# Kernel optimization log

Measured on AMD Instinct MI355X. Metric: run time of the kernel, lower is better.

The kernel has to match this reference:

```python
import jax, jax.numpy as jnp
import numpy as np
import math

B, S, INP = 64, 512, 64
D, H, L, DFF, LAT = 512, 8, 2, 2048, 128
SPARSE = 0.1  # sparse_factor default used by TransformerEncoderLayer


def _ln(x, g, b, eps=1e-5):
    m = x.mean(-1, keepdims=True)
    v = ((x - m) ** 2).mean(-1, keepdims=True)
    return (x - m) / jnp.sqrt(v + eps) * g + b


def _pe(s, d):
    pos = jnp.arange(s, dtype=jnp.float32)[:, None]
    div = jnp.exp(jnp.arange(0, d, 2, dtype=jnp.float32) * (-math.log(10000.0) / d))
    pe = jnp.zeros((s, d), dtype=jnp.float32)
    return pe.at[:, 0::2].set(jnp.sin(pos * div)).at[:, 1::2].set(jnp.cos(pos * div))


def _attn(h, g1, b1, wq, wk, wv, woW, wob):
    # h: (S, B, d). Faithful to source: transpose(1,2) yields (S, H, B, dk),
    # so attention is computed ACROSS THE BATCH axis at each timestep.
    s, bb, d = h.shape
    dk = d // H
    res = h
    hn = _ln(h, g1, b1)
    to_heads = lambda w: (hn @ w).reshape(s, bb, H, dk).swapaxes(1, 2)  # (S,H,B,dk)
    q, k, v = to_heads(wq), to_heads(wk), to_heads(wv)
    scores = jnp.einsum('shbd,shcd->shbc', q, k) / math.sqrt(dk)  # (S,H,B,B)
    kk = max(1, int(bb * SPARSE))  # topk row-sparsify before softmax
    thresh = jax.lax.top_k(scores, kk)[0][..., -1:]
    scores = jnp.where(scores >= thresh, scores, -1e9)
    w = jax.nn.softmax(scores, axis=-1)
    ctx = jnp.einsum('shbc,shcd->shbd', w, v).swapaxes(1, 2).reshape(s, bb, d)
    return ctx @ woW + wob + res


def _encoder(x, inW, inb, p):
    # x: (B, S, in_dim) -> (B, S, D)
    h = jnp.swapaxes(x, 0, 1)  # (S, B, in)
    h = (h @ inW + inb) * math.sqrt(D)
    h = h + _pe(h.shape[0], D)[:, None, :]
    for l in range(L):
        h = _attn(h, p['g1'][l], p['b1'][l], p['wq'][l], p['wk'][l], p['wv'][l], p['woW'][l], p['wob'][l])
        res = h
        f = _ln(h, p['g2'][l], p['b2'][l])
        f = jax.nn.gelu(f @ p['f1W'][l] + p['f1b'][l], approximate=False)
        h = f @ p['f2W'][l] + p['f2b'][l] + res
    h = _ln(h, p['gf'], p['bf'])
    return jnp.swapaxes(h, 0, 1)


_PKEYS = ['g1', 'b1', 'wq', 'wk', 'wv', 'woW', 'wob', 'g2', 'b2', 'f1W', 'f1b', 'f2W', 'f2b', 'gf', 'bf']


def _forward(x, enc_in_W, enc_in_b, enc_g1, enc_b1, enc_wq, enc_wk, enc_wv, enc_woW, enc_wob,
             enc_g2, enc_b2, enc_f1W, enc_f1b, enc_f2W, enc_f2b, enc_gf, enc_bf,
             mu_W, mu_b, lv_W, lv_b, dec_in_W, dec_in_b, dec_g1, dec_b1, dec_wq, dec_wk, dec_wv,
             dec_woW, dec_wob, dec_g2, dec_b2, dec_f1W, dec_f1b, dec_f2W, dec_f2b, dec_gf, dec_bf,
             out_W, out_b):
    enc_p = dict(zip(_PKEYS, [enc_g1, enc_b1, enc_wq, enc_wk, enc_wv, enc_woW, enc_wob, enc_g2, enc_b2, enc_f1W, enc_f1b, enc_f2W, enc_f2b, enc_gf, enc_bf]))
    dec_p = dict(zip(_PKEYS, [dec_g1, dec_b1, dec_wq, dec_wk, dec_wv, dec_woW, dec_wob, dec_g2, dec_b2, dec_f1W, dec_f1b, dec_f2W, dec_f2b, dec_gf, dec_bf]))
    enc_out = _encoder(x, enc_in_W, enc_in_b, enc_p)  # (B,S,D)
    pooled = enc_out.mean(axis=1)                      # (B,D)
    mu = pooled @ mu_W + mu_b
    logvar = pooled @ lv_W + lv_b
    z = mu  # eval mode: no reparameterization sampling
    z_seq = jnp.broadcast_to(z[:, None, :], (z.shape[0], S, LAT))
    dec_out = _encoder(z_seq, dec_in_W, dec_in_b, dec_p)
    recon = dec_out @ out_W + out_b
    return recon, mu, logvar


def setup_inputs() -> dict:
    key = jax.random.key(0)
    ks = iter(jax.random.split(key, 64))
    n = lambda shape, s=0.02: jax.random.normal(next(ks), shape, dtype=jnp.float32) * s

    def stack_params():
        return dict(
            g1=jnp.ones((L, D)), b1=jnp.zeros((L, D)),
            wq=n((L, D, D)), wk=n((L, D, D)), wv=n((L, D, D)),
            woW=n((L, D, D)), wob=jnp.zeros((L, D)),
            g2=jnp.ones((L, D)), b2=jnp.zeros((L, D)),
            f1W=n((L, D, DFF)), f1b=jnp.zeros((L, DFF)),
            f2W=n((L, DFF, D)), f2b=jnp.zeros((L, D)),
            gf=jnp.ones((D,)), bf=jnp.zeros((D,)))

    inp = {
        'x': jax.random.normal(next(ks), (B, S, INP), dtype=jnp.float32),
        'enc_in_W': n((INP, D), 0.05), 'enc_in_b': jnp.zeros((D,)),
        'mu_W': n((D, LAT), 0.05), 'mu_b': jnp.zeros((LAT,)),
        'lv_W': n((D, LAT), 0.05), 'lv_b': jnp.zeros((LAT,)),
        'dec_in_W': n((LAT, D), 0.05), 'dec_in_b': jnp.zeros((D,)),
        'out_W': n((D, INP), 0.05), 'out_b': jnp.zeros((INP,)),
    }
    for k_, v in stack_params().items():
        inp['enc_' + k_] = v
    for k_, v in stack_params().items():
        inp['dec_' + k_] = v
    return inp


def reference(x, enc_in_W, enc_in_b, enc_g1, enc_b1, enc_wq, enc_wk, enc_wv, enc_woW, enc_wob,
              enc_g2, enc_b2, enc_f1W, enc_f1b, enc_f2W, enc_f2b, enc_gf, enc_bf,
              mu_W, mu_b, lv_W, lv_b, dec_in_W, dec_in_b, dec_g1, dec_b1, dec_wq, dec_wk, dec_wv,
              dec_woW, dec_wob, dec_g2, dec_b2, dec_f1W, dec_f1b, dec_f2W, dec_f2b, dec_gf, dec_bf,
              out_W, out_b):
    return _forward(x, enc_in_W, enc_in_b, enc_g1, enc_b1, enc_wq, enc_wk, enc_wv, enc_woW, enc_wob,
                    enc_g2, enc_b2, enc_f1W, enc_f1b, enc_f2W, enc_f2b, enc_gf, enc_bf,
                    mu_W, mu_b, lv_W, lv_b, dec_in_W, dec_in_b, dec_g1, dec_b1, dec_wq, dec_wk, dec_wv,
                    dec_woW, dec_wob, dec_g2, dec_b2, dec_f1W, dec_f1b, dec_f2W, dec_f2b, dec_gf, dec_bf,
                    out_W, out_b)
```

## Files before the change

### kernel.cpp

```cpp
#include <hip/hip_runtime.h>
#include <math.h>


#define SQRT_D 22.62741699796952f
#define PE_C   0.017988946039015984f

typedef short frag8 __attribute__((ext_vector_type(8)));
typedef float accf4 __attribute__((ext_vector_type(4)));

#define GLL16(g, l) __builtin_amdgcn_global_load_lds( \
    (const __attribute__((address_space(1))) void*)(g), \
    (__attribute__((address_space(3))) void*)(l), 16, 0, 0)

__device__ __forceinline__ float bf2f(unsigned short u) {
    union { unsigned i; float f; } v; v.i = ((unsigned)u) << 16; return v.f;
}
__device__ __forceinline__ unsigned short f2bf(float f) {
    union { float f; unsigned i; } v; v.f = f;
    unsigned r = v.i + 0x7fff + ((v.i >> 16) & 1);
    return (unsigned short)(r >> 16);
}
__device__ __forceinline__ float pe_val(int s, int d) {
    float div = expf(-(float)(d & ~1) * PE_C);
    float ang = (float)s * div;
    return (d & 1) ? cosf(ang) : sinf(ang);
}
__device__ __forceinline__ float gelu_exact(float x) {
    return 0.5f * x * (1.0f + erff(x * 0.7071067811865476f));
}
__device__ __forceinline__ float gelu_fast(float x) {
    float xs = x * 0.7071067811865476f;
    float ax = fabsf(xs);
    float t  = 1.0f / (1.0f + 0.3275911f * ax);
    float p  = t * (0.254829592f + t * (-0.284496736f + t * (1.421413741f +
               t * (-1.453152027f + t * 1.061405429f))));
    float er = 1.0f - p * __expf(-ax * ax);
    er = (xs < 0.0f) ? -er : er;
    return 0.5f * x * (1.0f + er);
}

__device__ __forceinline__ void phase_bar() {
    __builtin_amdgcn_sched_barrier(0);
    __builtin_amdgcn_s_barrier();
    __builtin_amdgcn_sched_barrier(0);
}

__global__ __launch_bounds__(256) void pe_k(float* __restrict__ pe)
{
    const int s = blockIdx.x;
    const int d = threadIdx.x;
    pe[s * 512 + d]       = pe_val(s, d);
    pe[s * 512 + d + 256] = pe_val(s, d + 256);
}

__global__ __launch_bounds__(256) void embed_gemm_k(
    const float* __restrict__ x, const float* __restrict__ W,
    const float* __restrict__ bias, const float* __restrict__ pe,
    float* __restrict__ h)
{
    __shared__ float As[64][68];
    __shared__ float Ws[64][68];
    const int s = blockIdx.y;
    const int col0 = blockIdx.x * 64;
    const int tid = threadIdx.x;
#pragma unroll
    for (int i = 0; i < 16; i++) {
        int idx = i * 256 + tid;
        int r = idx >> 6, kk = idx & 63;
        As[kk][r] = x[((size_t)r * 512 + s) * 64 + kk];
        Ws[r][kk] = W[(size_t)r * 512 + col0 + kk];
    }
    __syncthreads();
    const int tm = (tid >> 4) << 2;
    const int tn = (tid & 15) << 2;
    float acc[4][4] = {};
#pragma unroll 8
    for (int kk = 0; kk < 64; kk++) {
        float4 a4 = *reinterpret_cast<const float4*>(&As[kk][tm]);
        float4 b4 = *reinterpret_cast<const float4*>(&Ws[kk][tn]);
        const float a[4] = {a4.x, a4.y, a4.z, a4.w};
        const float b[4] = {b4.x, b4.y, b4.z, b4.w};
#pragma unroll
        for (int i = 0; i < 4; i++)
#pragma unroll
            for (int j = 0; j < 4; j++)
                acc[i][j] += a[i] * b[j];
    }
    const int c = col0 + tn;
    float4 bi = *reinterpret_cast<const float4*>(&bias[c]);
    float4 pp = *reinterpret_cast<const float4*>(&pe[s * 512 + c]);
#pragma unroll
    for (int i = 0; i < 4; i++) {
        size_t row = ((size_t)s * 64 + tm + i) * 512;
        float4 o;
        o.x = (acc[i][0] + bi.x) * SQRT_D + pp.x;
        o.y = (acc[i][1] + bi.y) * SQRT_D + pp.y;
        o.z = (acc[i][2] + bi.z) * SQRT_D + pp.z;
        o.w = (acc[i][3] + bi.w) * SQRT_D + pp.w;
        *reinterpret_cast<float4*>(&h[row + c]) = o;
    }
}

__global__ __launch_bounds__(256) void dec_embed_k(
    const float* __restrict__ zemb, const float* __restrict__ pe,
    float* __restrict__ h)
{
    const int i4 = (blockIdx.x * 256 + threadIdx.x) * 4;
    const int d = i4 & 511;
    const int t = i4 >> 9;
    const int s = t >> 6, b = t & 63;
    float4 z = *reinterpret_cast<const float4*>(&zemb[b * 512 + d]);
    float4 p = *reinterpret_cast<const float4*>(&pe[s * 512 + d]);
    float4 o;
    o.x = z.x * SQRT_D + p.x;
    o.y = z.y * SQRT_D + p.y;
    o.z = z.z * SQRT_D + p.z;
    o.w = z.w * SQRT_D + p.w;
    *reinterpret_cast<float4*>(&h[i4]) = o;
}

__global__ __launch_bounds__(256) void stats_k(
    const float* __restrict__ x, float* __restrict__ st)
{
    const int row = blockIdx.x;
    const int tid = threadIdx.x;
    const float* xr = x + (size_t)row * 512;
    float2 vv = *reinterpret_cast<const float2*>(&xr[tid * 2]);
    float v0 = vv.x, v1 = vv.y;
    float ssum = v0 + v1;
#pragma unroll
    for (int off = 32; off > 0; off >>= 1) ssum += __shfl_down(ssum, off, 64);
    __shared__ float red[4];
    __shared__ float red2[4];
    const int wid = tid >> 6, lane = tid & 63;
    if (lane == 0) red[wid] = ssum;
    __syncthreads();
    float m = (red[0] + red[1] + red[2] + red[3]) * (1.f / 512.f);
    float d0 = v0 - m, d1 = v1 - m;
    float s2 = d0 * d0 + d1 * d1;
#pragma unroll
    for (int off = 32; off > 0; off >>= 1) s2 += __shfl_down(s2, off, 64);
    if (lane == 0) red2[wid] = s2;
    __syncthreads();
    if (tid == 0) {
        float var = (red2[0] + red2[1] + red2[2] + red2[3]) * (1.f / 512.f);
        st[row * 2]     = m;
        st[row * 2 + 1] = rsqrtf(var + 1e-5f);
    }
}

__global__ __launch_bounds__(256) void cast_ln_k(
    const float* __restrict__ x, const float* __restrict__ g,
    const float* __restrict__ b, unsigned short* __restrict__ y)
{
    const int row = blockIdx.x;
    const int tid = threadIdx.x;
    const float* xr = x + (size_t)row * 512;
    float2 vv = *reinterpret_cast<const float2*>(&xr[tid * 2]);
    float v0 = vv.x, v1 = vv.y;
    float ssum = v0 + v1;
#pragma unroll
    for (int off = 32; off > 0; off >>= 1) ssum += __shfl_down(ssum, off, 64);
    __shared__ float red[4];
    __shared__ float red2[4];
    const int wid = tid >> 6, lane = tid & 63;
    if (lane == 0) red[wid] = ssum;
    __syncthreads();
    float m = (red[0] + red[1] + red[2] + red[3]) * (1.f / 512.f);
    float d0 = v0 - m, d1 = v1 - m;
    float s2 = d0 * d0 + d1 * d1;
#pragma unroll
    for (int off = 32; off > 0; off >>= 1) s2 += __shfl_down(s2, off, 64);
    if (lane == 0) red2[wid] = s2;
    __syncthreads();
    float var = (red2[0] + red2[1] + red2[2] + red2[3]) * (1.f / 512.f);
    float rstd = rsqrtf(var + 1e-5f);
    float2 gg = *reinterpret_cast<const float2*>(&g[tid * 2]);
    float2 bb = *reinterpret_cast<const float2*>(&b[tid * 2]);
    ushort2 o;
    o.x = f2bf(d0 * rstd * gg.x + bb.x);
    o.y = f2bf(d1 * rstd * gg.y + bb.y);
    *reinterpret_cast<ushort2*>(&y[(size_t)row * 512 + tid * 2]) = o;
}

struct WTDesc { const float* src; unsigned short* dst; int Kd; int Nd; };

__global__ __launch_bounds__(256) void wtcast6_k(
    WTDesc d0, WTDesc d1, WTDesc d2, WTDesc d3, WTDesc d4, WTDesc d5)
{
    WTDesc d;
    switch (blockIdx.z) {
        case 0: d = d0; break; case 1: d = d1; break; case 2: d = d2; break;
        case 3: d = d3; break; case 4: d = d4; break; default: d = d5; break;
    }
    const int n0 = blockIdx.x * 32, k0 = blockIdx.y * 32;
    if (n0 >= d.Nd || k0 >= d.Kd) return;
    __shared__ float t[32][33];
    const int tx = threadIdx.x & 31, ty = threadIdx.x >> 5;
#pragma unroll
    for (int i = 0; i < 32; i += 8)
        t[ty + i][tx] = d.src[(size_t)(k0 + ty + i) * d.Nd + (n0 + tx)];
    __syncthreads();
#pragma unroll
    for (int i = 0; i < 32; i += 8)
        d.dst[(size_t)(n0 + ty + i) * d.Kd + (k0 + tx)] = f2bf(t[tx][ty + i]);
}

template<int ACT, int OUTBF, int RES, int BIAS>
__global__ __launch_bounds__(256, 2) void mgemm128_k(
    const unsigned short* __restrict__ A, int lda,
    const unsigned short* __restrict__ Bt, int ldb,
    const float* __restrict__ bias,
    const float* res, float* Cf, unsigned short* Cb, int ldc, int K)
{
    __shared__ unsigned short sm[32768];
    const int tid = threadIdx.x;
    const int wave = tid >> 6, lane = tid & 63;
    const int row0 = blockIdx.x * 128;
    const int col0 = blockIdx.y * 128;
    const int wr = wave >> 1, wc = wave & 1;
    const int wrbase = wr * 64, wcbase = wc * 64;
    const int frow = lane & 15;
    const int fcol = (lane >> 4) * 8;
    const int fxorE = (lane & 7) << 3;
    const int ccol = ((lane & 7) ^ (lane >> 3)) * 8;

    const int NT = K >> 6;

    auto stageA = [&](int buf, int k0t) {
#pragma unroll
        for (int i = 0; i < 4; i++) {
            int chunk = wave * 4 + i;
            GLL16(A + (size_t)(row0 + chunk * 8 + (lane >> 3)) * lda + k0t + ccol,
                  &sm[buf * 16384 + chunk * 512]);
        }
    };
    auto stageB = [&](int buf, int k0t) {
#pragma unroll
        for (int i = 0; i < 4; i++) {
            int chunk = wave * 4 + i;
            GLL16(Bt + (size_t)(col0 + chunk * 8 + (lane >> 3)) * ldb + k0t + ccol,
                  &sm[buf * 16384 + 8192 + chunk * 512]);
        }
    };

    accf4 acc[4][4] = {};
    frag8 af0[4], af1[4], bfr[4][2];

    stageA(0, 0); stageB(0, 0);
    if (NT > 1) { stageA(1, 64); stageB(1, 64); }
    if (NT > 1) asm volatile("s_waitcnt vmcnt(8)");
    else        asm volatile("s_waitcnt vmcnt(0)");
    phase_bar();

    for (int t = 0; t < NT; ++t) {
        const int ab = (t & 1) * 16384;
        const int bb = ab + 8192;
        const bool pf = (t + 2) < NT;
        const int kpf = (t + 2) << 6;

#pragma unroll
        for (int mi = 0; mi < 4; mi++)
            af0[mi] = *(const frag8*)&sm[ab + (wrbase + mi * 16 + frow) * 64 + (fcol ^ fxorE)];
#pragma unroll
        for (int nj = 0; nj < 4; nj++)
#pragma unroll
            for (int ks = 0; ks < 2; ks++)
                bfr[nj][ks] = *(const frag8*)&sm[bb + (wcbase + nj * 16 + frow) * 64 + ((ks * 32 + fcol) ^ fxorE)];
        phase_bar();
        __builtin_amdgcn_s_setprio(1);
#pragma unroll
        for (int mi = 0; mi < 4; mi++)
#pragma unroll
            for (int nj = 0; nj < 4; nj++)
                acc[mi][nj] = __builtin_amdgcn_mfma_f32_16x16x32_bf16(
                    bfr[nj][0], af0[mi], acc[mi][nj], 0, 0, 0);
        __builtin_amdgcn_s_setprio(0);
        phase_bar();

#pragma unroll
        for (int mi = 0; mi < 4; mi++)
            af1[mi] = *(const frag8*)&sm[ab + (wrbase + mi * 16 + frow) * 64 + ((32 + fcol) ^ fxorE)];
        if (pf) stageB(t & 1, kpf);
        phase_bar();
        __builtin_amdgcn_s_setprio(1);
#pragma unroll
        for (int mi = 0; mi < 4; mi++)
#pragma unroll
            for (int nj = 0; nj < 4; nj++)
                acc[mi][nj] = __builtin_amdgcn_mfma_f32_16x16x32_bf16(
                    bfr[nj][1], af1[mi], acc[mi][nj], 0, 0, 0);
        __builtin_amdgcn_s_setprio(0);
        if (pf) stageA(t & 1, kpf);
        if (pf) asm volatile("s_waitcnt vmcnt(8)");
        else    asm volatile("s_waitcnt vmcnt(0)");
        phase_bar();
    }

    const int lrow = lane & 15;
    const int lcol = (lane >> 4) * 4;
#pragma unroll
    for (int mi = 0; mi < 4; mi++) {
        const int r = row0 + wrbase + mi * 16 + lrow;
#pragma unroll
        for (int nj = 0; nj < 4; nj++) {
            const int c = col0 + wcbase + nj * 16 + lcol;
            float4 v = make_float4(acc[mi][nj][0], acc[mi][nj][1],
                                   acc[mi][nj][2], acc[mi][nj][3]);
            if (BIAS) {
                float4 bi = *reinterpret_cast<const float4*>(&bias[c]);
                v.x += bi.x; v.y += bi.y; v.z += bi.z; v.w += bi.w;
            }
            if (ACT) {
                v.x = gelu_fast(v.x); v.y = gelu_fast(v.y);
                v.z = gelu_fast(v.z); v.w = gelu_fast(v.w);
            }
            if (RES) {
                float4 rr = *reinterpret_cast<const float4*>(&res[(size_t)r * ldc + c]);
                v.x += rr.x; v.y += rr.y; v.z += rr.z; v.w += rr.w;
            }
            if (OUTBF) {
                ushort4 o;
                o.x = f2bf(v.x); o.y = f2bf(v.y); o.z = f2bf(v.z); o.w = f2bf(v.w);
                *reinterpret_cast<ushort4*>(&Cb[(size_t)r * ldc + c]) = o;
            } else {
                *reinterpret_cast<float4*>(&Cf[(size_t)r * ldc + c]) = v;
            }
        }
    }
}

__global__ __launch_bounds__(256) void attn2_k(
    const unsigned short* __restrict__ qkv, unsigned short* __restrict__ ctx)
{
    __shared__ float QT[64][68];
    __shared__ float KT[64][68];
    __shared__ float Vs[64][68];
    const int blk = blockIdx.x;
    const int sl = blk >> 3, hh = blk & 7;
    const int tid = threadIdx.x;
    const size_t qbase = (size_t)sl * 64 * 1536 + (size_t)hh * 64;
#pragma unroll
    for (int i = 0; i < 16; i++) {
        int idx = i * 256 + tid;
        int rr = idx >> 6, cc = idx & 63;
        const size_t g = qbase + (size_t)rr * 1536 + cc;
        QT[cc][rr] = bf2f(qkv[g]);
        KT[cc][rr] = bf2f(qkv[g + 512]);
        Vs[rr][cc] = bf2f(qkv[g + 1024]);
    }
    __syncthreads();
    const int tm = (tid >> 4) << 2;
    const int tn = (tid & 15) << 2;
    float sc[4][4] = {};
#pragma unroll 4
    for (int kk = 0; kk < 64; kk++) {
        float4 a4 = *reinterpret_cast<const float4*>(&QT[kk][tm]);
        float4 b4 = *reinterpret_cast<const float4*>(&KT[kk][tn]);
        const float a[4] = {a4.x, a4.y, a4.z, a4.w};
        const float b[4] = {b4.x, b4.y, b4.z, b4.w};
#pragma unroll
        for (int i = 0; i < 4; i++)
#pragma unroll
            for (int j = 0; j < 4; j++)
                sc[i][j] += a[i] * b[j];
    }
    __syncthreads();
    float (*ScT)[68] = KT;
#pragma unroll
    for (int i = 0; i < 4; i++)
#pragma unroll
        for (int j = 0; j < 4; j++)
            ScT[tn + j][tm + i] = sc[i][j] * 0.125f;
    __syncthreads();
    const int row = tid & 63, seg = tid >> 6;
    float* candp = &QT[0][0];
    {
        float top[6];
#pragma unroll
        for (int i = 0; i < 6; i++) top[i] = -3.4e38f;
#pragma unroll
        for (int c = seg * 16; c < seg * 16 + 16; c++) {
            float vv = ScT[c][row];
            if (vv > top[5]) {
                top[5] = vv;
#pragma unroll
                for (int i = 5; i > 0; i--)
                    if (top[i] > top[i - 1]) { float t = top[i]; top[i] = top[i - 1]; top[i - 1] = t; }
            }
        }
#pragma unroll
        for (int i = 0; i < 6; i++) candp[row * 24 + seg * 6 + i] = top[i];
    }
    __syncthreads();
    if (seg == 0) {
        float t6[6];
#pragma unroll
        for (int i = 0; i < 6; i++) t6[i] = -3.4e38f;
#pragma unroll
        for (int j = 0; j < 24; j++) {
            float vv = candp[row * 24 + j];
            if (vv > t6[5]) {
                t6[5] = vv;
#pragma unroll
                for (int i = 5; i > 0; i--)
                    if (t6[i] > t6[i - 1]) { float t = t6[i]; t6[i] = t6[i - 1]; t6[i - 1] = t; }
            }
        }
        ScT[row][64] = t6[5];
        ScT[row][65] = t6[0];
    }
    __syncthreads();
    {
        const float thresh = ScT[row][64], mx = ScT[row][65];
        float dsum = 0.f;
#pragma unroll
        for (int c = seg * 16; c < seg * 16 + 16; c++) {
            float vv = ScT[c][row];
            float w = (vv >= thresh) ? expf(vv - mx) : 0.f;
            dsum += w;
            QT[c][row] = w;
        }
        Vs[row][64 + seg] = dsum;
    }
    __syncthreads();
    {
        const float rd = 1.f / (Vs[row][64] + Vs[row][65] + Vs[row][66] + Vs[row][67]);
#pragma unroll
        for (int c = seg * 16; c < seg * 16 + 16; c++) QT[c][row] *= rd;
    }
    __syncthreads();
    {
        float acc[4][4] = {};
#pragma unroll 4
        for (int c = 0; c < 64; c++) {
            float4 p4 = *reinterpret_cast<const float4*>(&QT[c][tm]);
            float4 v4 = *reinterpret_cast<const float4*>(&Vs[c][tn]);
            const float p[4] = {p4.x, p4.y, p4.z, p4.w};
            const float b[4] = {v4.x, v4.y, v4.z, v4.w};
#pragma unroll
            for (int i = 0; i < 4; i++)
#pragma unroll
                for (int j = 0; j < 4; j++)
                    acc[i][j] += p[i] * b[j];
        }
#pragma unroll
        for (int i = 0; i < 4; i++) {
            ushort4 o;
            o.x = f2bf(acc[i][0]); o.y = f2bf(acc[i][1]);
            o.z = f2bf(acc[i][2]); o.w = f2bf(acc[i][3]);
            *reinterpret_cast<ushort4*>(
                &ctx[(size_t)(sl * 64 + tm + i) * 512 + hh * 64 + tn]) = o;
        }
    }
}

template<int ACT, int PERM, int LN>
__global__ __launch_bounds__(256) void gemm_k(
    const float* __restrict__ A, int lda,
    const float* __restrict__ W, int ldw,
    const float* __restrict__ bias,
    const float* res,
    float* C, int ldc,
    int K,
    const float* __restrict__ stats,
    const float* __restrict__ lng, const float* __restrict__ lnb)
{
    __shared__ float As[16][68];
    __shared__ float Ws[16][68];
    __shared__ float ms[64], rss[64];
    const int row0 = blockIdx.y * 64;
    const int col0 = blockIdx.x * 64;
    const int tid = threadIdx.x;
    if (LN) {
        if (tid < 64) {
            ms[tid]  = stats[(row0 + tid) * 2];
            rss[tid] = stats[(row0 + tid) * 2 + 1];
        }
        __syncthreads();
    }
    const int tm = (tid >> 4) << 2;
    const int tn = (tid & 15) << 2;
    float acc[4][4] = {};
    for (int k0 = 0; k0 < K; k0 += 16) {
#pragma unroll
        for (int i = 0; i < 4; i++) {
            int idx = i * 256 + tid;
            int r = idx >> 4, kk = idx & 15;
            float v = A[(size_t)(row0 + r) * lda + (k0 + kk)];
            if (LN) v = (v - ms[r]) * rss[r] * lng[k0 + kk] + lnb[k0 + kk];
            As[kk][r] = v;
        }
#pragma unroll
        for (int i = 0; i < 4; i++) {
            int idx = i * 256 + tid;
            int kk = idx >> 6, c = idx & 63;
            Ws[kk][c] = W[(size_t)(k0 + kk) * ldw + (col0 + c)];
        }
        __syncthreads();
#pragma unroll
        for (int kk = 0; kk < 16; kk++) {
            float4 a4 = *reinterpret_cast<const float4*>(&As[kk][tm]);
            float4 b4 = *reinterpret_cast<const float4*>(&Ws[kk][tn]);
            const float a[4] = {a4.x, a4.y, a4.z, a4.w};
            const float b[4] = {b4.x, b4.y, b4.z, b4.w};
#pragma unroll
            for (int i = 0; i < 4; i++)
#pragma unroll
                for (int j = 0; j < 4; j++)
                    acc[i][j] += a[i] * b[j];
        }
        __syncthreads();
    }
#pragma unroll
    for (int i = 0; i < 4; i++) {
        int r = row0 + tm + i;
#pragma unroll
        for (int j = 0; j < 4; j++) {
            int c = col0 + tn + j;
            float v = acc[i][j];
            if (bias) v += bias[c];
            if (ACT == 1) v = gelu_exact(v);
            if (res) v += res[(size_t)r * ldc + c];
            if (PERM) {
                int bb = r & 63, ss = r >> 6;
                C[((size_t)bb * 512 + ss) * ldc + c] = v;
            } else {
                C[(size_t)r * ldc + c] = v;
            }
        }
    }
}

__global__ __launch_bounds__(512) void pool_ln_k(
    const float* __restrict__ h, const float* __restrict__ st,
    const float* __restrict__ gf, const float* __restrict__ bf,
    float* __restrict__ pooled)
{
    const int b = blockIdx.x;
    const int d = threadIdx.x;
    const float g = gf[d], bb = bf[d];
    float acc = 0.f;
    for (int s = 0; s < 512; s++) {
        int r = s * 64 + b;
        float m = st[r * 2], rs = st[r * 2 + 1];
        acc += (h[(size_t)r * 512 + d] - m) * rs * g + bb;
    }
    pooled[b * 512 + d] = acc * (1.f / 512.f);
}

static void run_layer2(const float* const* p, int l,
                       float* h, unsigned short* hn_bf,
                       unsigned short* qkv, int chunk_rows,
                       unsigned short* f1c, int cw,
                       unsigned short* wqkv_t, unsigned short* wo_t,
                       unsigned short* f1_t, unsigned short* f2_t,
                       hipStream_t stream)
{
    const float* g1  = p[0] + l * 512;
    const float* b1  = p[1] + l * 512;
    const float* wq  = p[2] + (size_t)l * 262144;
    const float* wk  = p[3] + (size_t)l * 262144;
    const float* wv  = p[4] + (size_t)l * 262144;
    const float* wo  = p[5] + (size_t)l * 262144;
    const float* wob = p[6] + l * 512;
    const float* g2  = p[7] + l * 512;
    const float* b2  = p[8] + l * 512;
    const float* f1W = p[9] + (size_t)l * 1048576;
    const float* f1b = p[10] + l * 2048;
    const float* f2W = p[11] + (size_t)l * 1048576;
    const float* f2b = p[12] + l * 512;

    {
        WTDesc d0 = {wq,  wqkv_t,          512,  512};
        WTDesc d1 = {wk,  wqkv_t + 262144, 512,  512};
        WTDesc d2 = {wv,  wqkv_t + 524288, 512,  512};
        WTDesc d3 = {wo,  wo_t,            512,  512};
        WTDesc d4 = {f1W, f1_t,            512,  2048};
        WTDesc d5 = {f2W, f2_t,            2048, 512};
        wtcast6_k<<<dim3(64, 64, 6), 256, 0, stream>>>(d0, d1, d2, d3, d4, d5);
    }

    cast_ln_k<<<32768, 256, 0, stream>>>(h, g1, b1, hn_bf);
    for (int r0 = 0; r0 < 32768; r0 += chunk_rows) {
        mgemm128_k<0, 1, 0, 0><<<dim3(chunk_rows / 128, 12), 256, 0, stream>>>(
            hn_bf + (size_t)r0 * 512, 512, wqkv_t, 512, nullptr,
            nullptr, nullptr, qkv, 1536, 512);
        attn2_k<<<(chunk_rows / 64) * 8, 256, 0, stream>>>(
            qkv, hn_bf + (size_t)r0 * 512);
    }
    mgemm128_k<0, 0, 1, 1><<<dim3(256, 4), 256, 0, stream>>>(
        hn_bf, 512, wo_t, 512, wob, h, h, nullptr, 512, 512);

    cast_ln_k<<<32768, 256, 0, stream>>>(h, g2, b2, hn_bf);
    for (int c0 = 0; c0 < 2048; c0 += cw) {
        mgemm128_k<1, 1, 0, 1><<<dim3(256, cw / 128), 256, 0, stream>>>(
            hn_bf, 512, f1_t + (size_t)c0 * 512, 512, f1b + c0,
            nullptr, nullptr, f1c, cw, 512);
        if (c0 == 0)
            mgemm128_k<0, 0, 1, 1><<<dim3(256, 4), 256, 0, stream>>>(
                f1c, cw, f2_t + c0, 2048, f2b, h, h, nullptr, 512, cw);
        else
            mgemm128_k<0, 0, 1, 0><<<dim3(256, 4), 256, 0, stream>>>(
                f1c, cw, f2_t + c0, 2048, nullptr, h, h, nullptr, 512, cw);
    }
}

extern "C" void kernel_launch(void* const* d_in, const int* in_sizes, int n_in,
                              void* d_out, int out_size, void* d_ws, size_t ws_size,
                              hipStream_t stream)
{
    const float* x       = (const float*)d_in[0];
    const float* enc_inW = (const float*)d_in[1];
    const float* enc_inb = (const float*)d_in[2];
    const float* mu_W    = (const float*)d_in[3];
    const float* mu_b    = (const float*)d_in[4];
    const float* lv_W    = (const float*)d_in[5];
    const float* lv_b    = (const float*)d_in[6];
    const float* dec_inW = (const float*)d_in[7];
    const float* dec_inb = (const float*)d_in[8];
    const float* out_W   = (const float*)d_in[9];
    const float* out_b   = (const float*)d_in[10];
    const float* const* ep = (const float* const*)(d_in + 11);
    const float* const* dp = (const float* const*)(d_in + 26);

    float* fout   = (float*)d_out;
    float* mu_out = fout + 2097152;
    float* lv_out = mu_out + 8192;

    const size_t SZ = (size_t)32768 * 512;
    size_t off = 0;
    char* base = (char*)d_ws;
    auto take = [&](size_t bytes) -> char* {
        char* pp = base + off;
        off = (off + bytes + 255) & ~(size_t)255;
        return pp;
    };
    float*          h      = (float*)take(SZ * 4);
    unsigned short* hn_bf  = (unsigned short*)take(SZ * 2);
    unsigned short* wqkv_t = (unsigned short*)take(1536 * 512 * 2);
    unsigned short* wo_t   = (unsigned short*)take(512 * 512 * 2);
    unsigned short* f1_t   = (unsigned short*)take(2048 * 512 * 2);
    unsigned short* f2_t   = (unsigned short*)take(512 * 2048 * 2);
    float*          stats  = (float*)take(65536 * 4);
    float*          pooled = (float*)take(131072);
    float*          zemb   = (float*)take(131072);
    float*          pe     = (float*)take(512 * 512 * 4);

    unsigned short* qkv; unsigned short* f1c;
    int chunk_rows, cw;
    size_t rem = (ws_size > off) ? (ws_size - off) : 0;
    const size_t F1_FULL  = (size_t)32768 * 2048 * 2;
    const size_t QKV_FULL = (size_t)32768 * 1536 * 2;
    if (rem >= F1_FULL + 512) {
        unsigned short* share = (unsigned short*)take(F1_FULL);
        qkv = share; f1c = share; chunk_rows = 32768; cw = 2048;
    } else if (rem >= QKV_FULL + 512) {
        unsigned short* share = (unsigned short*)take(QKV_FULL);
        qkv = share; f1c = share; chunk_rows = 32768; cw = 512;
    } else if (rem >= (size_t)32768 * 512 * 2 + 512) {
        unsigned short* share = (unsigned short*)take((size_t)32768 * 512 * 2);
        qkv = share; f1c = share; chunk_rows = 8192; cw = 512;
    } else {
        qkv = (unsigned short*)take((size_t)4096 * 1536 * 2);
        chunk_rows = 4096;
        f1c = (unsigned short*)fout; cw = 128;
    }

    const int M = 32768;

    pe_k<<<512, 256, 0, stream>>>(pe);

    embed_gemm_k<<<dim3(8, 512), 256, 0, stream>>>(x, enc_inW, enc_inb, pe, h);
    for (int l = 0; l < 2; l++)
        run_layer2(ep, l, h, hn_bf, qkv, chunk_rows, f1c, cw,
                   wqkv_t, wo_t, f1_t, f2_t, stream);

    stats_k<<<M, 256, 0, stream>>>(h, stats);
    pool_ln_k<<<64, 512, 0, stream>>>(h, stats, ep[13], ep[14], pooled);
    gemm_k<0, 0, 0><<<dim3(2, 1), 256, 0, stream>>>(pooled, 512, mu_W, 128, mu_b,
                                                    nullptr, mu_out, 128, 512,
                                                    nullptr, nullptr, nullptr);
    gemm_k<0, 0, 0><<<dim3(2, 1), 256, 0, stream>>>(pooled, 512, lv_W, 128, lv_b,
                                                    nullptr, lv_out, 128, 512,
                                                    nullptr, nullptr, nullptr);
    gemm_k<0, 0, 0><<<dim3(8, 1), 256, 0, stream>>>(mu_out, 128, dec_inW, 512, dec_inb,
                                                    nullptr, zemb, 512, 128,
                                                    nullptr, nullptr, nullptr);
    dec_embed_k<<<16384, 256, 0, stream>>>(zemb, pe, h);

    for (int l = 0; l < 2; l++)
        run_layer2(dp, l, h, hn_bf, qkv, chunk_rows, f1c, cw,
                   wqkv_t, wo_t, f1_t, f2_t, stream);

    stats_k<<<M, 256, 0, stream>>>(h, stats);
    gemm_k<0, 1, 1><<<dim3(1, M / 64), 256, 0, stream>>>(
        h, 512, out_W, 64, out_b, nullptr, fout, 64, 512, stats, dp[13], dp[14]);
}
```

Measured before the change: 2.367 ms.

## Use MFMA for batch attention, remap GEMM blocks per XCD, restructure k-loop

The per-timestep attention kernel now stores Q, K and V^T in swizzled bf16 shared memory and computes QK^T and PV with bf16 MFMA instructions, replacing the scalar fp32 FMA loops. The normalization is applied in the epilogue, and the softmax weights are rounded to bf16 before they are summed. The 128x128 GEMM remaps block indices so each XCD covers a contiguous band of rows, aiming for better L2 reuse. Its k-loop loads both k-halves of the fragments at once, issues the next tile's prefetch before the MFMAs, and uses one barrier pair per tile instead of two. The risks are bf16 precision loss in the attention probabilities and more register pressure from the larger fragment arrays.

```diff
diff --git a/kernel.cpp b/kernel.cpp
--- a/kernel.cpp
+++ b/kernel.cpp
@@ -216,8 +216,21 @@
     __shared__ unsigned short sm[32768];
     const int tid = threadIdx.x;
     const int wave = tid >> 6, lane = tid & 63;
-    const int row0 = blockIdx.x * 128;
-    const int col0 = blockIdx.y * 128;
+
+    int bx = blockIdx.x, by = blockIdx.y;
+    if (gridDim.x == 256) {
+        const int id = blockIdx.x + (blockIdx.y << 8);
+        const int span = gridDim.y << 4;
+        const int xcd = id & 7;
+        const int q = id >> 3;
+        const int hb = q / span;
+        const int r2 = q - hb * span;
+        bx = (xcd << 5) + (hb << 4) + (r2 & 15);
+        by = r2 >> 4;
+    }
+    const int row0 = bx * 128;
+    const int col0 = by * 128;
+
     const int wr = wave >> 1, wc = wave & 1;
     const int wrbase = wr * 64, wcbase = wc * 64;
     const int frow = lane & 15;
@@ -245,12 +258,12 @@
     };
 
     accf4 acc[4][4] = {};
-    frag8 af0[4], af1[4], bfr[4][2];
+    frag8 af[4][2], bfr[4][2];
 
     stageA(0, 0); stageB(0, 0);
     if (NT > 1) { stageA(1, 64); stageB(1, 64); }
-    if (NT > 1) asm volatile("s_waitcnt vmcnt(8)");
-    else        asm volatile("s_waitcnt vmcnt(0)");
+    if (NT > 1) asm volatile("s_waitcnt vmcnt(8)" ::: "memory");
+    else        asm volatile("s_waitcnt vmcnt(0)" ::: "memory");
     phase_bar();
 
     for (int t = 0; t < NT; ++t) {
@@ -261,39 +274,30 @@
 
 #pragma unroll
         for (int mi = 0; mi < 4; mi++)
-            af0[mi] = *(const frag8*)&sm[ab + (wrbase + mi * 16 + frow) * 64 + (fcol ^ fxorE)];
+#pragma unroll
+            for (int ks = 0; ks < 2; ks++)
+                af[mi][ks] = *(const frag8*)&sm[ab + (wrbase + mi * 16 + frow) * 64 + ((ks * 32 + fcol) ^ fxorE)];
 #pragma unroll
         for (int nj = 0; nj < 4; nj++)
 #pragma unroll
             for (int ks = 0; ks < 2; ks++)
                 bfr[nj][ks] = *(const frag8*)&sm[bb + (wcbase + nj * 16 + frow) * 64 + ((ks * 32 + fcol) ^ fxorE)];
+        asm volatile("s_waitcnt lgkmcnt(0)" ::: "memory");
         phase_bar();
+
+        if (pf) { stageB(t & 1, kpf); stageA(t & 1, kpf); }
         __builtin_amdgcn_s_setprio(1);
 #pragma unroll
         for (int mi = 0; mi < 4; mi++)
 #pragma unroll
             for (int nj = 0; nj < 4; nj++)
-                acc[mi][nj] = __builtin_amdgcn_mfma_f32_16x16x32_bf16(
-                    bfr[nj][0], af0[mi], acc[mi][nj], 0, 0, 0);
+#pragma unroll
+                for (int ks = 0; ks < 2; ks++)
+                    acc[mi][nj] = __builtin_amdgcn_mfma_f32_16x16x32_bf16(
+                        bfr[nj][ks], af[mi][ks], acc[mi][nj], 0, 0, 0);
         __builtin_amdgcn_s_setprio(0);
-        phase_bar();
-
-#pragma unroll
-        for (int mi = 0; mi < 4; mi++)
-            af1[mi] = *(const frag8*)&sm[ab + (wrbase + mi * 16 + frow) * 64 + ((32 + fcol) ^ fxorE)];
-        if (pf) stageB(t & 1, kpf);
-        phase_bar();
-        __builtin_amdgcn_s_setprio(1);
-#pragma unroll
-        for (int mi = 0; mi < 4; mi++)
-#pragma unroll
-            for (int nj = 0; nj < 4; nj++)
-                acc[mi][nj] = __builtin_amdgcn_mfma_f32_16x16x32_bf16(
-                    bfr[nj][1], af1[mi], acc[mi][nj], 0, 0, 0);
-        __builtin_amdgcn_s_setprio(0);
-        if (pf) stageA(t & 1, kpf);
-        if (pf) asm volatile("s_waitcnt vmcnt(8)");
-        else    asm volatile("s_waitcnt vmcnt(0)");
+        if (pf) asm volatile("s_waitcnt vmcnt(8)" ::: "memory");
+        else    asm volatile("s_waitcnt vmcnt(0)" ::: "memory");
         phase_bar();
     }
 
@@ -330,51 +334,77 @@
     }
 }
 
-__global__ __launch_bounds__(256) void attn2_k(
+__global__ __launch_bounds__(256) void attn3_k(
     const unsigned short* __restrict__ qkv, unsigned short* __restrict__ ctx)
 {
-    __shared__ float QT[64][68];
-    __shared__ float KT[64][68];
-    __shared__ float Vs[64][68];
+    __shared__ unsigned short QL[4096];
+    __shared__ unsigned short KL[4096];
+    __shared__ unsigned short VT[4096];
+    __shared__ float ScT[64][68];
+    __shared__ float dsums[64][4];
+    __shared__ float rds[64];
     const int blk = blockIdx.x;
     const int sl = blk >> 3, hh = blk & 7;
     const int tid = threadIdx.x;
+    const int wave = tid >> 6, lane = tid & 63;
     const size_t qbase = (size_t)sl * 64 * 1536 + (size_t)hh * 64;
-#pragma unroll
-    for (int i = 0; i < 16; i++) {
-        int idx = i * 256 + tid;
-        int rr = idx >> 6, cc = idx & 63;
-        const size_t g = qbase + (size_t)rr * 1536 + cc;
-        QT[cc][rr] = bf2f(qkv[g]);
-        KT[cc][rr] = bf2f(qkv[g + 512]);
-        Vs[rr][cc] = bf2f(qkv[g + 1024]);
-    }
-    __syncthreads();
-    const int tm = (tid >> 4) << 2;
-    const int tn = (tid & 15) << 2;
-    float sc[4][4] = {};
-#pragma unroll 4
-    for (int kk = 0; kk < 64; kk++) {
-        float4 a4 = *reinterpret_cast<const float4*>(&QT[kk][tm]);
-        float4 b4 = *reinterpret_cast<const float4*>(&KT[kk][tn]);
-        const float a[4] = {a4.x, a4.y, a4.z, a4.w};
-        const float b[4] = {b4.x, b4.y, b4.z, b4.w};
-#pragma unroll
-        for (int i = 0; i < 4; i++)
-#pragma unroll
-            for (int j = 0; j < 4; j++)
-                sc[i][j] += a[i] * b[j];
-    }
-    __syncthreads();
-    float (*ScT)[68] = KT;
-#pragma unroll
-    for (int i = 0; i < 4; i++)
-#pragma unroll
-        for (int j = 0; j < 4; j++)
-            ScT[tn + j][tm + i] = sc[i][j] * 0.125f;
-    __syncthreads();
+
+    {
+        const int r = tid >> 2;
+        const int dg = (tid & 3) << 4;
+        const int x = (r & 7) << 3;
+        const unsigned short* gp = qkv + qbase + (size_t)r * 1536 + dg;
+        frag8 q0 = *(const frag8*)(gp);
+        frag8 q1 = *(const frag8*)(gp + 8);
+        frag8 k0 = *(const frag8*)(gp + 512);
+        frag8 k1 = *(const frag8*)(gp + 520);
+        frag8 v0 = *(const frag8*)(gp + 1024);
+        frag8 v1 = *(const frag8*)(gp + 1032);
+        *(frag8*)&QL[r * 64 + (dg ^ x)]       = q0;
+        *(frag8*)&QL[r * 64 + ((dg + 8) ^ x)] = q1;
+        *(frag8*)&KL[r * 64 + (dg ^ x)]       = k0;
+        *(frag8*)&KL[r * 64 + ((dg + 8) ^ x)] = k1;
+#pragma unroll
+        for (int i = 0; i < 16; i++) {
+            int ii = (i + r) & 15;
+            int j = dg + ii;
+            unsigned short e = (unsigned short)(ii < 8 ? v0[ii] : v1[ii - 8]);
+            VT[j * 64 + (r ^ ((j & 7) << 3))] = e;
+        }
+    }
+    __syncthreads();
+
+    const int frow = lane & 15;
+    const int fcol8 = (lane >> 4) * 8;
+    const int fx = (lane & 7) << 3;
+
+    {
+        const int c0 = wave * 16;
+        accf4 sacc[4] = {};
+#pragma unroll
+        for (int ks = 0; ks < 2; ks++) {
+            frag8 kf = *(const frag8*)&KL[(c0 + frow) * 64 + ((ks * 32 + fcol8) ^ fx)];
+#pragma unroll
+            for (int rt = 0; rt < 4; rt++) {
+                frag8 qf = *(const frag8*)&QL[(rt * 16 + frow) * 64 + ((ks * 32 + fcol8) ^ fx)];
+                sacc[rt] = __builtin_amdgcn_mfma_f32_16x16x32_bf16(
+                    qf, kf, sacc[rt], 0, 0, 0);
+            }
+        }
+        const int cc = c0 + frow;
+        const int rb = (lane >> 4) * 4;
+#pragma unroll
+        for (int rt = 0; rt < 4; rt++) {
+            float4 s4;
+            s4.x = sacc[rt][0] * 0.125f; s4.y = sacc[rt][1] * 0.125f;
+            s4.z = sacc[rt][2] * 0.125f; s4.w = sacc[rt][3] * 0.125f;
+            *(float4*)&ScT[cc][rt * 16 + rb] = s4;
+        }
+    }
+    __syncthreads();
+
     const int row = tid & 63, seg = tid >> 6;
-    float* candp = &QT[0][0];
+    float* candp = (float*)&KL[0];
     {
         float top[6];
 #pragma unroll
@@ -413,44 +443,46 @@
     __syncthreads();
     {
         const float thresh = ScT[row][64], mx = ScT[row][65];
+        const int xr = (row & 7) << 3;
         float dsum = 0.f;
 #pragma unroll
         for (int c = seg * 16; c < seg * 16 + 16; c++) {
             float vv = ScT[c][row];
             float w = (vv >= thresh) ? expf(vv - mx) : 0.f;
-            dsum += w;
-            QT[c][row] = w;
-        }
-        Vs[row][64 + seg] = dsum;
-    }
-    __syncthreads();
+            unsigned short wb = f2bf(w);
+            dsum += bf2f(wb);
+            QL[row * 64 + (c ^ xr)] = wb;
+        }
+        dsums[row][seg] = dsum;
+    }
+    __syncthreads();
+    if (tid < 64)
+        rds[tid] = 1.f / (dsums[tid][0] + dsums[tid][1] + dsums[tid][2] + dsums[tid][3]);
+    __syncthreads();
+
     {
-        const float rd = 1.f / (Vs[row][64] + Vs[row][65] + Vs[row][66] + Vs[row][67]);
-#pragma unroll
-        for (int c = seg * 16; c < seg * 16 + 16; c++) QT[c][row] *= rd;
-    }
-    __syncthreads();
-    {
-        float acc[4][4] = {};
-#pragma unroll 4
-        for (int c = 0; c < 64; c++) {
-            float4 p4 = *reinterpret_cast<const float4*>(&QT[c][tm]);
-            float4 v4 = *reinterpret_cast<const float4*>(&Vs[c][tn]);
-            const float p[4] = {p4.x, p4.y, p4.z, p4.w};
-            const float b[4] = {v4.x, v4.y, v4.z, v4.w};
-#pragma unroll
-            for (int i = 0; i < 4; i++)
-#pragma unroll
-                for (int j = 0; j < 4; j++)
-                    acc[i][j] += p[i] * b[j];
-        }
-#pragma unroll
-        for (int i = 0; i < 4; i++) {
+        const int r0 = wave * 16;
+        accf4 pacc[4] = {};
+#pragma unroll
+        for (int ks = 0; ks < 2; ks++) {
+            frag8 pf = *(const frag8*)&QL[(r0 + frow) * 64 + ((ks * 32 + fcol8) ^ fx)];
+#pragma unroll
+            for (int jt = 0; jt < 4; jt++) {
+                frag8 vf = *(const frag8*)&VT[(jt * 16 + frow) * 64 + ((ks * 32 + fcol8) ^ fx)];
+                pacc[jt] = __builtin_amdgcn_mfma_f32_16x16x32_bf16(
+                    vf, pf, pacc[jt], 0, 0, 0);
+            }
+        }
+        const int rr = r0 + frow;
+        const int jb = (lane >> 4) * 4;
+        const float sc = rds[rr];
+#pragma unroll
+        for (int jt = 0; jt < 4; jt++) {
             ushort4 o;
-            o.x = f2bf(acc[i][0]); o.y = f2bf(acc[i][1]);
-            o.z = f2bf(acc[i][2]); o.w = f2bf(acc[i][3]);
+            o.x = f2bf(pacc[jt][0] * sc); o.y = f2bf(pacc[jt][1] * sc);
+            o.z = f2bf(pacc[jt][2] * sc); o.w = f2bf(pacc[jt][3] * sc);
             *reinterpret_cast<ushort4*>(
-                &ctx[(size_t)(sl * 64 + tm + i) * 512 + hh * 64 + tn]) = o;
+                &ctx[(size_t)(sl * 64 + rr) * 512 + hh * 64 + jt * 16 + jb]) = o;
         }
     }
 }
@@ -586,7 +618,7 @@
         mgemm128_k<0, 1, 0, 0><<<dim3(chunk_rows / 128, 12), 256, 0, stream>>>(
             hn_bf + (size_t)r0 * 512, 512, wqkv_t, 512, nullptr,
             nullptr, nullptr, qkv, 1536, 512);
-        attn2_k<<<(chunk_rows / 64) * 8, 256, 0, stream>>>(
+        attn3_k<<<(chunk_rows / 64) * 8, 256, 0, stream>>>(
             qkv, hn_bf + (size_t)r0 * 512);
     }
     mgemm128_k<0, 0, 1, 1><<<dim3(256, 4), 256, 0, stream>>>(
```

Result: faster. 2.042 ms (-13.7%).
